# Optimization experiments

Hardware: AMD Instinct MI355X
Metric: run time of the kernel (lower is better)

## Reference

```python
import jax, jax.numpy as jnp
import numpy as np

N_LAYER, D_MODEL, D_INNER, D_STATE, DT_RANK, D_CONV = 4, 256, 512, 16, 16, 4
IN_FEAT, OUT_DIM, MID, NCLS, B, L = 64, 128, 50, 3, 16, 1024


def setup_inputs() -> dict:
    key = jax.random.key(0)
    ks = jax.random.split(key, 16)
    def lin(k, out_f, in_f, extra=()):  # stacked linear weights, fan_in scaled
        return jax.random.normal(k, extra + (out_f, in_f), jnp.float32) / np.sqrt(in_f)
    nl = (N_LAYER,)
    inp = {
        "x": jax.random.normal(ks[0], (B, L, IN_FEAT), jnp.float32),
        "emb_W": lin(ks[1], D_MODEL, IN_FEAT),
        "emb_b": jnp.zeros((D_MODEL,), jnp.float32),
        "in_W": lin(ks[2], 2 * D_INNER, D_MODEL, nl),
        "conv_W": jax.random.normal(ks[3], (N_LAYER, D_INNER, 1, D_CONV), jnp.float32) / np.sqrt(D_CONV),
        "conv_b": jnp.zeros((N_LAYER, D_INNER), jnp.float32),
        "xp_W": lin(ks[4], DT_RANK + 2 * D_STATE, D_INNER, nl),
        "dt_W": lin(ks[5], D_INNER, DT_RANK, nl),
        "dt_b": jnp.full((N_LAYER, D_INNER), -4.6, jnp.float32),  # softplus ~ 0.01
        "A_log": jnp.broadcast_to(jnp.log(jnp.arange(1, D_STATE + 1, dtype=jnp.float32)), (N_LAYER, D_INNER, D_STATE)),
        "Dp": jnp.ones((N_LAYER, D_INNER), jnp.float32),
        "out_W": lin(ks[6], D_MODEL, D_INNER, nl),
        "norm_W": jnp.ones((N_LAYER, D_MODEL), jnp.float32),
        "normf_W": jnp.ones((D_MODEL,), jnp.float32),
        "head_W": lin(ks[7], OUT_DIM, D_MODEL),
        "head_b": jnp.zeros((OUT_DIM,), jnp.float32),
        "W1": lin(ks[8], MID, OUT_DIM),
        "b1": jnp.zeros((MID,), jnp.float32),
        "W2": lin(ks[9], NCLS, MID),
        "b2": jnp.zeros((NCLS,), jnp.float32),
    }
    return inp


def _rmsnorm(x, w, eps=1e-5):
    return x * jax.lax.rsqrt(jnp.mean(x * x, axis=-1, keepdims=True) + eps) * w


def _causal_dwconv(x, w, b):  # x [B,L,D], w [D,1,K]
    xt = jnp.transpose(x, (0, 2, 1))  # [B,D,L]
    y = jax.lax.conv_general_dilated(
        xt, w, window_strides=(1,), padding=[(w.shape[-1] - 1, 0)],
        dimension_numbers=("NCH", "OIH", "NCH"), feature_group_count=xt.shape[1])
    return jnp.transpose(y, (0, 2, 1)) + b


def _selective_scan(dA, dBu, C):  # dA,dBu [B,L,D,N], C [B,L,N] -> y [B,L,D]
    dA_t = jnp.moveaxis(dA, 1, 0)
    dBu_t = jnp.moveaxis(dBu, 1, 0)
    C_t = jnp.moveaxis(C, 1, 0)
    h0 = jnp.zeros(dA.shape[:1] + dA.shape[2:], dA.dtype)  # [B,D,N]
    def step(h, inp):
        a, bu, c = inp
        h = a * h + bu
        return h, jnp.einsum("bdn,bn->bd", h, c)
    _, ys = jax.lax.scan(step, h0, (dA_t, dBu_t, C_t))
    return jnp.moveaxis(ys, 0, 1)


def _mamba_block(h, in_W, conv_W, conv_b, xp_W, dt_W, dt_b, A_log, Dp, out_W):
    xr = jnp.einsum("bld,ed->ble", h, in_W)  # [B,L,2*D_INNER]
    xm, res = jnp.split(xr, 2, axis=-1)
    xs = jax.nn.silu(_causal_dwconv(xm, conv_W, conv_b))
    dbc = jnp.einsum("bld,ed->ble", xs, xp_W)
    dlt, Bm, Cm = jnp.split(dbc, [DT_RANK, DT_RANK + D_STATE], axis=-1)
    delta = jax.nn.softplus(jnp.einsum("blr,dr->bld", dlt, dt_W) + dt_b)  # [B,L,D]
    A = -jnp.exp(A_log)  # [D,N]
    dA = jnp.exp(jnp.einsum("bld,dn->bldn", delta, A))
    dBu = jnp.einsum("bld,bln,bld->bldn", delta, Bm, xs)
    y = _selective_scan(dA, dBu, Cm) + xs * Dp
    y = y * jax.nn.silu(res)
    return jnp.einsum("bld,ed->ble", y, out_W)


def reference(x, emb_W, emb_b, in_W, conv_W, conv_b, xp_W, dt_W, dt_b, A_log,
              Dp, out_W, norm_W, normf_W, head_W, head_b, W1, b1, W2, b2):
    h = jnp.einsum("blf,df->bld", x, emb_W) + emb_b  # project to d_model
    for i in range(N_LAYER):
        h = h + _mamba_block(_rmsnorm(h, norm_W[i]), in_W[i], conv_W[i], conv_b[i],
                             xp_W[i], dt_W[i], dt_b[i], A_log[i], Dp[i], out_W[i])
    h = _rmsnorm(h, normf_W)
    feat = jnp.mean(jnp.einsum("bld,od->blo", h, head_W) + head_b, axis=1)  # [B,out_dim]
    hid = jax.nn.relu(feat @ W1.T + b1)
    return hid @ W2.T + b2  # [B, class_num] logits
```

## Files before the change

### kernel.cpp

```cpp
#include <hip/hip_runtime.h>
#include <math.h>

#define NL 4
#define DM 256
#define DI 512
#define DSTATE 16
#define DTRANK 16
#define DCONV 4
#define IN_FEAT 64
#define OUT_DIM 128
#define MID 50
#define NCLS 3
#define BB 16
#define LL 1024
#define T_TOK (BB*LL)
#define CHUNK 32
#define NCH (LL/CHUNK)

typedef short bf8_t __attribute__((ext_vector_type(8)));
typedef float f32x4 __attribute__((ext_vector_type(4)));

__device__ __forceinline__ float silu_f(float x) {
    return x / (1.f + __expf(-x));
}
__device__ __forceinline__ float softplus_f(float x) {
    return (x > 20.f) ? x : log1pf(__expf(x));
}
__device__ __forceinline__ unsigned short f2bf_rne(float f) {
    unsigned int u = __float_as_uint(f);
    unsigned int r = (u + 0x7FFFu + ((u >> 16) & 1u)) >> 16;
    return (unsigned short)r;
}
__device__ __forceinline__ float bf2f(unsigned short s) {
    return __uint_as_float(((unsigned int)s) << 16);
}
__device__ __forceinline__ void split_bf(float v, unsigned short& hi, unsigned short& lo) {
    unsigned short h = f2bf_rne(v);
    hi = h;
    lo = f2bf_rne(v - bf2f(h));
}
__device__ __forceinline__ void glds16(const unsigned short* g, unsigned short* l) {
    __builtin_amdgcn_global_load_lds(
        (const __attribute__((address_space(1))) void*)g,
        (__attribute__((address_space(3))) void*)l, 16, 0, 0);
}

template<int ACT, bool ACC, bool BIAS, bool SPLIT>
__global__ __launch_bounds__(256, 2)
void gemm_bf16x3(const unsigned short* __restrict__ Ahi,
                 const unsigned short* __restrict__ Alo,
                 const unsigned short* __restrict__ Whi,
                 const unsigned short* __restrict__ Wlo,
                 const float* __restrict__ bias,
                 float* __restrict__ C0, int ldc0,
                 float* __restrict__ C1, int ldc1, int NS,
                 int M, int N, int K)
{
    __shared__ __align__(16) unsigned short lds[4][128][32];

    const int tid = threadIdx.x;
    const int lane = tid & 63;
    const int bm = blockIdx.y * 128;
    const int bn = blockIdx.x * 128;
    const int wid = tid >> 6;
    const int wr = wid >> 1;
    const int wc = wid & 1;

    f32x4 acc[4][4];
    #pragma unroll
    for (int i = 0; i < 4; ++i)
        #pragma unroll
        for (int j = 0; j < 4; ++j)
            acc[i][j] = (f32x4){0.f, 0.f, 0.f, 0.f};

    const int l15 = lane & 15;
    const int kc  = lane >> 4;

    const int u0 = tid, u1 = tid + 256;
    const int r0 = u0 >> 2, s0 = (u0 & 3) ^ ((u0 >> 3) & 3);
    const int r1 = u1 >> 2, s1 = (u1 & 3) ^ ((u1 >> 3) & 3);

    for (int k0 = 0; k0 < K; k0 += 32) {
        __syncthreads();
        {
            const size_t ga0 = (size_t)(bm + r0) * K + k0 + s0 * 8;
            const size_t ga1 = (size_t)(bm + r1) * K + k0 + s1 * 8;
            const size_t gb0 = (size_t)(bn + r0) * K + k0 + s0 * 8;
            const size_t gb1 = (size_t)(bn + r1) * K + k0 + s1 * 8;
            glds16(Ahi + ga0, &lds[0][0][0] + u0 * 8);
            glds16(Ahi + ga1, &lds[0][0][0] + u1 * 8);
            glds16(Alo + ga0, &lds[1][0][0] + u0 * 8);
            glds16(Alo + ga1, &lds[1][0][0] + u1 * 8);
            glds16(Whi + gb0, &lds[2][0][0] + u0 * 8);
            glds16(Whi + gb1, &lds[2][0][0] + u1 * 8);
            glds16(Wlo + gb0, &lds[3][0][0] + u0 * 8);
            glds16(Wlo + gb1, &lds[3][0][0] + u1 * 8);
        }
        asm volatile("s_waitcnt vmcnt(0)" ::: "memory");
        __syncthreads();

        bf8_t ah[4], al[4], bh[4], bl[4];
        #pragma unroll
        for (int mi = 0; mi < 4; ++mi) {
            const int r = wr * 64 + mi * 16 + l15;
            const int sl = kc ^ ((r >> 1) & 3);
            ah[mi] = *(bf8_t*)&lds[0][r][sl * 8];
            al[mi] = *(bf8_t*)&lds[1][r][sl * 8];
        }
        #pragma unroll
        for (int nj = 0; nj < 4; ++nj) {
            const int r = wc * 64 + nj * 16 + l15;
            const int sl = kc ^ ((r >> 1) & 3);
            bh[nj] = *(bf8_t*)&lds[2][r][sl * 8];
            bl[nj] = *(bf8_t*)&lds[3][r][sl * 8];
        }

        #pragma unroll
        for (int mi = 0; mi < 4; ++mi)
            #pragma unroll
            for (int nj = 0; nj < 4; ++nj) {
                acc[mi][nj] = __builtin_amdgcn_mfma_f32_16x16x32_bf16(
                    ah[mi], bh[nj], acc[mi][nj], 0, 0, 0);
                acc[mi][nj] = __builtin_amdgcn_mfma_f32_16x16x32_bf16(
                    ah[mi], bl[nj], acc[mi][nj], 0, 0, 0);
                acc[mi][nj] = __builtin_amdgcn_mfma_f32_16x16x32_bf16(
                    al[mi], bh[nj], acc[mi][nj], 0, 0, 0);
            }
    }

    #pragma unroll
    for (int mi = 0; mi < 4; ++mi) {
        const int row0 = bm + wr * 64 + mi * 16 + (lane >> 4) * 4;
        #pragma unroll
        for (int nj = 0; nj < 4; ++nj) {
            const int col = bn + wc * 64 + nj * 16 + l15;
            float bv = BIAS ? bias[col] : 0.f;
            #pragma unroll
            for (int r = 0; r < 4; ++r) {
                float val = acc[mi][nj][r] + bv;
                if (ACT == 1) val = softplus_f(val);
                const int m = row0 + r;
                float* dst;
                if (SPLIT && col >= NS) dst = C1 + (size_t)m * ldc1 + (col - NS);
                else                    dst = C0 + (size_t)m * ldc0 + col;
                if (ACC) *dst += val; else *dst = val;
            }
        }
    }
}

__global__ __launch_bounds__(256, 2)
void gemm_bf16x3_bc(const unsigned short* __restrict__ Ahi,
                    const unsigned short* __restrict__ Alo,
                    const unsigned short* __restrict__ Whi,
                    const unsigned short* __restrict__ Wlo,
                    float* __restrict__ C, int K)
{
    __shared__ __align__(16) unsigned short ldsA[2][128][32];
    __shared__ __align__(16) unsigned short ldsW[2][48][32];

    const int tid = threadIdx.x;
    const int lane = tid & 63;
    const int wid = tid >> 6;
    const int bm = blockIdx.x * 128;

    f32x4 acc[2][3];
    #pragma unroll
    for (int i = 0; i < 2; ++i)
        #pragma unroll
        for (int j = 0; j < 3; ++j)
            acc[i][j] = (f32x4){0.f, 0.f, 0.f, 0.f};

    const int l15 = lane & 15;
    const int kc  = lane >> 4;

    const int u0 = tid, u1 = tid + 256;
    const int r0 = u0 >> 2, s0 = (u0 & 3) ^ ((u0 >> 3) & 3);
    const int r1 = u1 >> 2, s1 = (u1 & 3) ^ ((u1 >> 3) & 3);

    for (int k0 = 0; k0 < K; k0 += 32) {
        __syncthreads();
        {
            const size_t ga0 = (size_t)(bm + r0) * K + k0 + s0 * 8;
            const size_t ga1 = (size_t)(bm + r1) * K + k0 + s1 * 8;
            glds16(Ahi + ga0, &ldsA[0][0][0] + u0 * 8);
            glds16(Ahi + ga1, &ldsA[0][0][0] + u1 * 8);
            glds16(Alo + ga0, &ldsA[1][0][0] + u0 * 8);
            glds16(Alo + ga1, &ldsA[1][0][0] + u1 * 8);
            if (tid < 192) {
                const size_t gw = (size_t)r0 * K + k0 + s0 * 8;
                glds16(Whi + gw, &ldsW[0][0][0] + u0 * 8);
                glds16(Wlo + gw, &ldsW[1][0][0] + u0 * 8);
            }
        }
        asm volatile("s_waitcnt vmcnt(0)" ::: "memory");
        __syncthreads();

        bf8_t ah[2], al[2], bh[3], bl[3];
        #pragma unroll
        for (int mi = 0; mi < 2; ++mi) {
            const int r = wid * 32 + mi * 16 + l15;
            const int sl = kc ^ ((r >> 1) & 3);
            ah[mi] = *(bf8_t*)&ldsA[0][r][sl * 8];
            al[mi] = *(bf8_t*)&ldsA[1][r][sl * 8];
        }
        #pragma unroll
        for (int nj = 0; nj < 3; ++nj) {
            const int r = nj * 16 + l15;
            const int sl = kc ^ ((r >> 1) & 3);
            bh[nj] = *(bf8_t*)&ldsW[0][r][sl * 8];
            bl[nj] = *(bf8_t*)&ldsW[1][r][sl * 8];
        }

        #pragma unroll
        for (int mi = 0; mi < 2; ++mi)
            #pragma unroll
            for (int nj = 0; nj < 3; ++nj) {
                acc[mi][nj] = __builtin_amdgcn_mfma_f32_16x16x32_bf16(
                    ah[mi], bh[nj], acc[mi][nj], 0, 0, 0);
                acc[mi][nj] = __builtin_amdgcn_mfma_f32_16x16x32_bf16(
                    ah[mi], bl[nj], acc[mi][nj], 0, 0, 0);
                acc[mi][nj] = __builtin_amdgcn_mfma_f32_16x16x32_bf16(
                    al[mi], bh[nj], acc[mi][nj], 0, 0, 0);
            }
    }

    #pragma unroll
    for (int mi = 0; mi < 2; ++mi) {
        const int row0 = bm + wid * 32 + mi * 16 + (lane >> 4) * 4;
        #pragma unroll
        for (int nj = 0; nj < 3; ++nj) {
            const int col = nj * 16 + l15;
            #pragma unroll
            for (int r = 0; r < 4; ++r)
                C[(size_t)(row0 + r) * 48 + col] = acc[mi][nj][r];
        }
    }
}

__global__ __launch_bounds__(256)
void delta_kernel(const float* __restrict__ dbc, const float* __restrict__ dt_W,
                  const float* __restrict__ dt_b, float* __restrict__ delta)
{
    const int t = blockIdx.x;
    __shared__ float dl[16];
    if (threadIdx.x < 16) dl[threadIdx.x] = dbc[(size_t)t * 48 + threadIdx.x];
    __syncthreads();
    #pragma unroll
    for (int i = 0; i < 2; ++i) {
        const int d = threadIdx.x + i * 256;
        float s = dt_b[d];
        #pragma unroll
        for (int r = 0; r < 16; ++r)
            s = fmaf(dl[r], dt_W[d * 16 + r], s);
        delta[(size_t)t * DI + d] = softplus_f(s);
    }
}

template<int ACT, bool ACC>
__global__ __launch_bounds__(256)
void gemm_f32(const float* __restrict__ A, int lda,
              const float* __restrict__ Bw,
              const float* __restrict__ bias,
              float* __restrict__ C0, int ldc0,
              float* __restrict__ C1, int ldc1, int NS,
              int M, int N, int K)
{
    __shared__ float As[64][16];
    __shared__ float Bs[16][65];

    const int tid = threadIdx.x;
    const int bm = blockIdx.y * 64;
    const int bn = blockIdx.x * 64;
    const int tx = tid & 15;
    const int ty = tid >> 4;

    float acc[4][4] = {};

    const int r  = tid >> 2;
    const int kk = (tid & 3) * 4;

    for (int k0 = 0; k0 < K; k0 += 16) {
        int ar = bm + r; if (ar >= M) ar = M - 1;
        float4 av = *(const float4*)(A + (size_t)ar * lda + k0 + kk);
        *(float4*)(&As[r][kk]) = av;

        int br = bn + r; if (br >= N) br = N - 1;
        float4 bv = *(const float4*)(Bw + (size_t)br * K + k0 + kk);
        Bs[kk + 0][r] = bv.x;
        Bs[kk + 1][r] = bv.y;
        Bs[kk + 2][r] = bv.z;
        Bs[kk + 3][r] = bv.w;

        __syncthreads();
        #pragma unroll
        for (int k = 0; k < 16; ++k) {
            float a[4], bvv[4];
            #pragma unroll
            for (int i = 0; i < 4; ++i) a[i] = As[ty * 4 + i][k];
            #pragma unroll
            for (int j = 0; j < 4; ++j) bvv[j] = Bs[k][tx * 4 + j];
            #pragma unroll
            for (int i = 0; i < 4; ++i)
                #pragma unroll
                for (int j = 0; j < 4; ++j)
                    acc[i][j] = fmaf(a[i], bvv[j], acc[i][j]);
        }
        __syncthreads();
    }

    #pragma unroll
    for (int i = 0; i < 4; ++i) {
        int m = bm + ty * 4 + i;
        if (m >= M) continue;
        #pragma unroll
        for (int j = 0; j < 4; ++j) {
            int n = bn + tx * 4 + j;
            if (n >= N) continue;
            float v = acc[i][j];
            if (bias) v += bias[n];
            if (ACT == 1) v = softplus_f(v);
            float* dst;
            if (n < NS) dst = C0 + (size_t)m * ldc0 + n;
            else        dst = C1 + (size_t)m * ldc1 + (n - NS);
            if (ACC) *dst += v; else *dst = v;
        }
    }
}

__global__ __launch_bounds__(256)
void split4_kernel(const float* __restrict__ src, unsigned short* __restrict__ hi,
                   unsigned short* __restrict__ lo, int n4)
{
    int i = blockIdx.x * 256 + threadIdx.x;
    if (i >= n4) return;
    float4 v = ((const float4*)src)[i];
    ushort4 h, l;
    split_bf(v.x, h.x, l.x);
    split_bf(v.y, h.y, l.y);
    split_bf(v.z, h.z, l.z);
    split_bf(v.w, h.w, l.w);
    ((ushort4*)hi)[i] = h;
    ((ushort4*)lo)[i] = l;
}

__global__ __launch_bounds__(256)
void rmsnorm_bf16_kernel(const float* __restrict__ x, const float* __restrict__ w,
                         unsigned short* __restrict__ hi, unsigned short* __restrict__ lo)
{
    const int wave = threadIdx.x >> 6;
    const int lane = threadIdx.x & 63;
    const int t = blockIdx.x * 4 + wave;
    const float* xp = x + (size_t)t * DM;
    float4 v = *(const float4*)(xp + lane * 4);
    float ss = v.x * v.x + v.y * v.y + v.z * v.z + v.w * v.w;
    #pragma unroll
    for (int off = 1; off < 64; off <<= 1) ss += __shfl_xor(ss, off);
    float inv = rsqrtf(ss * (1.f / DM) + 1e-5f);
    float4 wv = *(const float4*)(w + lane * 4);
    float o[4] = { v.x * inv * wv.x, v.y * inv * wv.y,
                   v.z * inv * wv.z, v.w * inv * wv.w };
    ushort4 h, l;
    split_bf(o[0], h.x, l.x);
    split_bf(o[1], h.y, l.y);
    split_bf(o[2], h.z, l.z);
    split_bf(o[3], h.w, l.w);
    *(ushort4*)(hi + (size_t)t * DM + lane * 4) = h;
    *(ushort4*)(lo + (size_t)t * DM + lane * 4) = l;
}

__global__ __launch_bounds__(256)
void rmsnorm_kernel(const float* __restrict__ x, const float* __restrict__ w,
                    float* __restrict__ out)
{
    const int wave = threadIdx.x >> 6;
    const int lane = threadIdx.x & 63;
    const int t = blockIdx.x * 4 + wave;
    const float* xp = x + (size_t)t * DM;
    float4 v = *(const float4*)(xp + lane * 4);
    float ss = v.x * v.x + v.y * v.y + v.z * v.z + v.w * v.w;
    #pragma unroll
    for (int off = 1; off < 64; off <<= 1) ss += __shfl_xor(ss, off);
    float inv = rsqrtf(ss * (1.f / DM) + 1e-5f);
    float4 wv = *(const float4*)(w + lane * 4);
    float4 o;
    o.x = v.x * inv * wv.x;
    o.y = v.y * inv * wv.y;
    o.z = v.z * inv * wv.z;
    o.w = v.w * inv * wv.w;
    *(float4*)(out + (size_t)t * DM + lane * 4) = o;
}

__global__ __launch_bounds__(256)
void conv_silu_kernel(const float* __restrict__ xm,
                      const float* __restrict__ w,
                      const float* __restrict__ cb,
                      float* __restrict__ xs,
                      unsigned short* __restrict__ xs_hi,
                      unsigned short* __restrict__ xs_lo)
{
    const int idx = blockIdx.x * 256 + threadIdx.x;
    const int d = idx & (DI - 1);
    const int t = idx >> 9;
    const int l = t & (LL - 1);
    float acc = cb[d];
    const float* wp = w + d * 4;
    #pragma unroll
    for (int k = 0; k < 4; ++k) {
        int ll = l + k - 3;
        if (ll >= 0) acc = fmaf(xm[(size_t)(t + k - 3) * DI + d], wp[k], acc);
    }
    float v = silu_f(acc);
    xs[idx] = v;
    unsigned short hh, lo;
    split_bf(v, hh, lo);
    xs_hi[idx] = hh;
    xs_lo[idx] = lo;
}

__global__ __launch_bounds__(256)
void scan_p1(const float* __restrict__ delta,
             const float* __restrict__ dbc,
             const float* __restrict__ xs,
             const float* __restrict__ A_log,
             float* __restrict__ st,
             float* __restrict__ sdl)
{
    const int blk = blockIdx.x;
    const int dhalf = blk & 1;
    const int chunk = (blk >> 1) & (NCH - 1);
    const int b = blk >> 6;
    const int d = (dhalf << 8) + threadIdx.x;
    const int t0 = b * LL + chunk * CHUNK;

    __shared__ float Bs[CHUNK][DSTATE];
    for (int i = threadIdx.x; i < CHUNK * DSTATE; i += 256) {
        int s = i >> 4, n = i & 15;
        Bs[s][n] = dbc[(size_t)(t0 + s) * 48 + 16 + n];
    }
    __syncthreads();

    float An[16];
    #pragma unroll
    for (int n = 0; n < 16; ++n) An[n] = -__expf(A_log[d * 16 + n]);

    float h[16];
    #pragma unroll
    for (int n = 0; n < 16; ++n) h[n] = 0.f;
    float sumdl = 0.f;

    for (int s = 0; s < CHUNK; ++s) {
        const size_t off = (size_t)(t0 + s) * DI + d;
        const float dl = delta[off];
        const float du = dl * xs[off];
        sumdl += dl;
        #pragma unroll
        for (int n = 0; n < 16; ++n) {
            float a = __expf(dl * An[n]);
            h[n] = fmaf(a, h[n], du * Bs[s][n]);
        }
    }

    const size_t base = ((size_t)(b * NCH + chunk) * DSTATE) * DI + d;
    #pragma unroll
    for (int n = 0; n < 16; ++n) st[base + (size_t)n * DI] = h[n];
    sdl[(size_t)(b * NCH + chunk) * DI + d] = sumdl;
}

__global__ __launch_bounds__(256)
void scan_p2(float* __restrict__ st, const float* __restrict__ sdl,
             const float* __restrict__ A_log)
{
    const int b = blockIdx.x >> 1;
    const int d = ((blockIdx.x & 1) << 8) + threadIdx.x;

    float An[16];
    #pragma unroll
    for (int n = 0; n < 16; ++n) An[n] = -__expf(A_log[d * 16 + n]);

    float H[16];
    #pragma unroll
    for (int n = 0; n < 16; ++n) H[n] = 0.f;

    for (int c = 0; c < NCH; ++c) {
        const size_t base = ((size_t)(b * NCH + c) * DSTATE) * DI + d;
        const float sums = sdl[(size_t)(b * NCH + c) * DI + d];
        #pragma unroll
        for (int n = 0; n < 16; ++n) {
            float fin = st[base + (size_t)n * DI];
            float dec = __expf(An[n] * sums);
            st[base + (size_t)n * DI] = H[n];
            H[n] = fmaf(dec, H[n], fin);
        }
    }
}

__global__ __launch_bounds__(256)
void scan_p3(const float* __restrict__ delta,
             const float* __restrict__ dbc,
             const float* __restrict__ xs,
             const float* __restrict__ res,
             const float* __restrict__ A_log,
             const float* __restrict__ Dp,
             const float* __restrict__ st,
             unsigned short* __restrict__ y_hi,
             unsigned short* __restrict__ y_lo)
{
    const int blk = blockIdx.x;
    const int dhalf = blk & 1;
    const int chunk = (blk >> 1) & (NCH - 1);
    const int b = blk >> 6;
    const int d = (dhalf << 8) + threadIdx.x;
    const int t0 = b * LL + chunk * CHUNK;

    __shared__ float BCs[CHUNK][32];
    for (int i = threadIdx.x; i < CHUNK * 32; i += 256) {
        int s = i >> 5, c = i & 31;
        BCs[s][c] = dbc[(size_t)(t0 + s) * 48 + 16 + c];
    }
    __syncthreads();

    float An[16];
    #pragma unroll
    for (int n = 0; n < 16; ++n) An[n] = -__expf(A_log[d * 16 + n]);
    const float Dv = Dp[d];

    const size_t base = ((size_t)(b * NCH + chunk) * DSTATE) * DI + d;
    float h[16];
    #pragma unroll
    for (int n = 0; n < 16; ++n) h[n] = st[base + (size_t)n * DI];

    for (int s = 0; s < CHUNK; ++s) {
        const size_t off = (size_t)(t0 + s) * DI + d;
        const float dl = delta[off];
        const float xv = xs[off];
        const float rv = res[off];
        const float du = dl * xv;
        float acc = 0.f;
        #pragma unroll
        for (int n = 0; n < 16; ++n) {
            float a = __expf(dl * An[n]);
            h[n] = fmaf(a, h[n], du * BCs[s][n]);
            acc  = fmaf(h[n], BCs[s][16 + n], acc);
        }
        float y = fmaf(xv, Dv, acc) * silu_f(rv);
        unsigned short hh, ll;
        split_bf(y, hh, ll);
        y_hi[off] = hh;
        y_lo[off] = ll;
    }
}

__global__ void zero_kernel(float* __restrict__ p, int n)
{
    int i = blockIdx.x * 256 + threadIdx.x;
    if (i < n) p[i] = 0.f;
}

__global__ __launch_bounds__(256)
void hmean_kernel(const float* __restrict__ hn, float* __restrict__ hmean)
{
    const int b = blockIdx.x >> 4;
    const int lc = blockIdx.x & 15;
    const int d = threadIdx.x;
    float s = 0.f;
    for (int l = lc * 64; l < lc * 64 + 64; ++l)
        s += hn[((size_t)(b * LL + l)) * DM + d];
    atomicAdd(&hmean[b * DM + d], s * (1.f / LL));
}

__global__ __launch_bounds__(256)
void mlp_kernel(const float* __restrict__ feat, const float* __restrict__ W1,
                const float* __restrict__ b1, const float* __restrict__ W2,
                const float* __restrict__ b2, float* __restrict__ out)
{
    __shared__ float hid[BB][MID + 2];
    const int tid = threadIdx.x;
    for (int idx = tid; idx < BB * MID; idx += 256) {
        int b = idx / MID, m = idx % MID;
        float s = b1[m];
        for (int k = 0; k < OUT_DIM; ++k)
            s = fmaf(feat[b * OUT_DIM + k], W1[m * OUT_DIM + k], s);
        hid[b][m] = fmaxf(s, 0.f);
    }
    __syncthreads();
    if (tid < BB * NCLS) {
        int b = tid / NCLS, c = tid % NCLS;
        float s = b2[c];
        for (int k = 0; k < MID; ++k)
            s = fmaf(hid[b][k], W2[c * MID + k], s);
        out[b * NCLS + c] = s;
    }
}

extern "C" void kernel_launch(void* const* d_in, const int* in_sizes, int n_in,
                              void* d_out, int out_size, void* d_ws, size_t ws_size,
                              hipStream_t stream)
{
    const float* x       = (const float*)d_in[0];
    const float* emb_W   = (const float*)d_in[1];
    const float* emb_b   = (const float*)d_in[2];
    const float* in_W    = (const float*)d_in[3];
    const float* conv_W  = (const float*)d_in[4];
    const float* conv_b  = (const float*)d_in[5];
    const float* xp_W    = (const float*)d_in[6];
    const float* dt_W    = (const float*)d_in[7];
    const float* dt_b    = (const float*)d_in[8];
    const float* A_log   = (const float*)d_in[9];
    const float* Dp      = (const float*)d_in[10];
    const float* out_W   = (const float*)d_in[11];
    const float* norm_W  = (const float*)d_in[12];
    const float* normf_W = (const float*)d_in[13];
    const float* head_W  = (const float*)d_in[14];
    const float* head_b  = (const float*)d_in[15];
    const float* W1      = (const float*)d_in[16];
    const float* b1      = (const float*)d_in[17];
    const float* W2      = (const float*)d_in[18];
    const float* b2      = (const float*)d_in[19];

    const size_t TM = (size_t)T_TOK * DM;
    const size_t TD = (size_t)T_TOK * DI;

    float* ws    = (float*)d_ws;
    float* h     = ws;
    float* hn    = h   + TM;
    float* xm    = hn  + TM;
    float* res   = xm  + TD;
    float* xs    = res + TD;
    float* dbc   = xs  + TD;
    float* sdl   = dbc + (size_t)T_TOK * 48;
    float* hmean = sdl + (size_t)BB * NCH * DI;
    float* feat  = hmean + BB * DM;
    float* planes = feat + BB * OUT_DIM;
    float* wplanes = planes + TD;

    float* delta = xm;
    float* st  = hn;

    unsigned short* y_hi  = (unsigned short*)planes;
    unsigned short* y_lo  = y_hi + TD;
    unsigned short* xs_hi = (unsigned short*)planes;
    unsigned short* xs_lo = xs_hi + TD;
    unsigned short* hn_hi = (unsigned short*)planes;
    unsigned short* hn_lo = hn_hi + TM;
    unsigned short* x_hi  = (unsigned short*)planes;
    unsigned short* x_lo  = x_hi + (size_t)T_TOK * IN_FEAT;

    unsigned short* wp      = (unsigned short*)wplanes;
    unsigned short* embW_hi = wp;
    unsigned short* embW_lo = embW_hi + (size_t)DM * IN_FEAT;
    unsigned short* inW_hi  = embW_lo + (size_t)DM * IN_FEAT;
    unsigned short* inW_lo  = inW_hi + (size_t)NL * 2 * DI * DM;
    unsigned short* outW_hi = inW_lo + (size_t)NL * 2 * DI * DM;
    unsigned short* outW_lo = outW_hi + (size_t)NL * DM * DI;
    unsigned short* xpW_hi  = outW_lo + (size_t)NL * DM * DI;
    unsigned short* xpW_lo  = xpW_hi + (size_t)NL * 48 * DI;

    dim3 blk(256);

    split4_kernel<<<(DM * IN_FEAT / 4 + 255) / 256, blk, 0, stream>>>(
        emb_W, embW_hi, embW_lo, DM * IN_FEAT / 4);
    split4_kernel<<<(NL * 2 * DI * DM / 4 + 255) / 256, blk, 0, stream>>>(
        in_W, inW_hi, inW_lo, NL * 2 * DI * DM / 4);
    split4_kernel<<<(NL * DM * DI / 4 + 255) / 256, blk, 0, stream>>>(
        out_W, outW_hi, outW_lo, NL * DM * DI / 4);
    split4_kernel<<<(NL * 48 * DI / 4 + 255) / 256, blk, 0, stream>>>(
        xp_W, xpW_hi, xpW_lo, NL * 48 * DI / 4);
    split4_kernel<<<(T_TOK * IN_FEAT / 4 + 255) / 256, blk, 0, stream>>>(
        x, x_hi, x_lo, T_TOK * IN_FEAT / 4);

    gemm_bf16x3<0, false, true, false><<<dim3(DM / 128, T_TOK / 128), blk, 0, stream>>>(
        x_hi, x_lo, embW_hi, embW_lo, emb_b,
        h, DM, h, DM, DM, T_TOK, DM, IN_FEAT);

    for (int i = 0; i < NL; ++i) {
        rmsnorm_bf16_kernel<<<T_TOK / 4, blk, 0, stream>>>(
            h, norm_W + i * DM, hn_hi, hn_lo);

        gemm_bf16x3<0, false, false, true><<<dim3(2 * DI / 128, T_TOK / 128), blk, 0, stream>>>(
            hn_hi, hn_lo,
            inW_hi + (size_t)i * 2 * DI * DM, inW_lo + (size_t)i * 2 * DI * DM,
            nullptr, xm, DI, res, DI, DI, T_TOK, 2 * DI, DM);

        conv_silu_kernel<<<(T_TOK * DI) / 256, blk, 0, stream>>>(
            xm, conv_W + (size_t)i * DI * DCONV, conv_b + i * DI, xs, xs_hi, xs_lo);

        gemm_bf16x3_bc<<<T_TOK / 128, blk, 0, stream>>>(
            xs_hi, xs_lo, xpW_hi + (size_t)i * 48 * DI, xpW_lo + (size_t)i * 48 * DI,
            dbc, DI);

        delta_kernel<<<T_TOK, blk, 0, stream>>>(
            dbc, dt_W + (size_t)i * DI * DTRANK, dt_b + i * DI, delta);

        const float* Al = A_log + (size_t)i * DI * DSTATE;
        scan_p1<<<BB * NCH * 2, blk, 0, stream>>>(delta, dbc, xs, Al, st, sdl);
        scan_p2<<<32, blk, 0, stream>>>(st, sdl, Al);
        scan_p3<<<BB * NCH * 2, blk, 0, stream>>>(delta, dbc, xs, res, Al,
                                                  Dp + i * DI, st, y_hi, y_lo);

        gemm_bf16x3<0, true, false, false><<<dim3(DM / 128, T_TOK / 128), blk, 0, stream>>>(
            y_hi, y_lo,
            outW_hi + (size_t)i * DM * DI, outW_lo + (size_t)i * DM * DI,
            nullptr, h, DM, h, DM, DM, T_TOK, DM, DI);
    }

    rmsnorm_kernel<<<T_TOK / 4, blk, 0, stream>>>(h, normf_W, hn);
    zero_kernel<<<(BB * DM + 255) / 256, blk, 0, stream>>>(hmean, BB * DM);
    hmean_kernel<<<256, blk, 0, stream>>>(hn, hmean);
    gemm_f32<0, false><<<dim3(2, 1), blk, 0, stream>>>(
        hmean, DM, head_W, head_b, feat, OUT_DIM, feat, OUT_DIM, OUT_DIM,
        BB, OUT_DIM, DM);
    mlp_kernel<<<1, blk, 0, stream>>>(feat, W1, b1, W2, b2, (float*)d_out);
}
```

Before: 1.216 ms.

## Fuse delta projection into scan kernels and drop fp32 xs buffer

```diff
diff --git a/kernel.cpp b/kernel.cpp
--- a/kernel.cpp
+++ b/kernel.cpp
@@ -16,6 +16,7 @@
 #define T_TOK (BB*LL)
 #define CHUNK 32
 #define NCH (LL/CHUNK)
+#define TCH 16
 
 typedef short bf8_t __attribute__((ext_vector_type(8)));
 typedef float f32x4 __attribute__((ext_vector_type(4)));
@@ -238,25 +239,6 @@
     }
 }
 
-__global__ __launch_bounds__(256)
-void delta_kernel(const float* __restrict__ dbc, const float* __restrict__ dt_W,
-                  const float* __restrict__ dt_b, float* __restrict__ delta)
-{
-    const int t = blockIdx.x;
-    __shared__ float dl[16];
-    if (threadIdx.x < 16) dl[threadIdx.x] = dbc[(size_t)t * 48 + threadIdx.x];
-    __syncthreads();
-    #pragma unroll
-    for (int i = 0; i < 2; ++i) {
-        const int d = threadIdx.x + i * 256;
-        float s = dt_b[d];
-        #pragma unroll
-        for (int r = 0; r < 16; ++r)
-            s = fmaf(dl[r], dt_W[d * 16 + r], s);
-        delta[(size_t)t * DI + d] = softplus_f(s);
-    }
-}
-
 template<int ACT, bool ACC>
 __global__ __launch_bounds__(256)
 void gemm_f32(const float* __restrict__ A, int lda,
@@ -395,34 +377,53 @@
 void conv_silu_kernel(const float* __restrict__ xm,
                       const float* __restrict__ w,
                       const float* __restrict__ cb,
-                      float* __restrict__ xs,
                       unsigned short* __restrict__ xs_hi,
                       unsigned short* __restrict__ xs_lo)
 {
-    const int idx = blockIdx.x * 256 + threadIdx.x;
-    const int d = idx & (DI - 1);
-    const int t = idx >> 9;
-    const int l = t & (LL - 1);
-    float acc = cb[d];
-    const float* wp = w + d * 4;
-    #pragma unroll
-    for (int k = 0; k < 4; ++k) {
-        int ll = l + k - 3;
-        if (ll >= 0) acc = fmaf(xm[(size_t)(t + k - 3) * DI + d], wp[k], acc);
-    }
-    float v = silu_f(acc);
-    xs[idx] = v;
-    unsigned short hh, lo;
-    split_bf(v, hh, lo);
-    xs_hi[idx] = hh;
-    xs_lo[idx] = lo;
-}
-
-__global__ __launch_bounds__(256)
-void scan_p1(const float* __restrict__ delta,
-             const float* __restrict__ dbc,
-             const float* __restrict__ xs,
+    const int t0 = blockIdx.x * TCH;
+    const int l0 = t0 & (LL - 1);
+    const int d0 = threadIdx.x * 2;
+
+    const float4 wa = *(const float4*)(w + (size_t)d0 * 4);
+    const float4 wb = *(const float4*)(w + (size_t)(d0 + 1) * 4);
+    const float cbA = cb[d0], cbB = cb[d0 + 1];
+
+    float2 x0, x1, x2;
+    if (l0) {
+        x0 = *(const float2*)(xm + (size_t)(t0 - 3) * DI + d0);
+        x1 = *(const float2*)(xm + (size_t)(t0 - 2) * DI + d0);
+        x2 = *(const float2*)(xm + (size_t)(t0 - 1) * DI + d0);
+    } else {
+        x0 = x1 = x2 = (float2){0.f, 0.f};
+    }
+
+    #pragma unroll
+    for (int s = 0; s < TCH; ++s) {
+        const int t = t0 + s;
+        const float2 x3 = *(const float2*)(xm + (size_t)t * DI + d0);
+        float aA = cbA, aB = cbB;
+        aA = fmaf(wa.x, x0.x, aA); aB = fmaf(wb.x, x0.y, aB);
+        aA = fmaf(wa.y, x1.x, aA); aB = fmaf(wb.y, x1.y, aB);
+        aA = fmaf(wa.z, x2.x, aA); aB = fmaf(wb.z, x2.y, aB);
+        aA = fmaf(wa.w, x3.x, aA); aB = fmaf(wb.w, x3.y, aB);
+        const float vA = silu_f(aA);
+        const float vB = silu_f(aB);
+        ushort2 h2, l2;
+        split_bf(vA, h2.x, l2.x);
+        split_bf(vB, h2.y, l2.y);
+        *(ushort2*)(xs_hi + (size_t)t * DI + d0) = h2;
+        *(ushort2*)(xs_lo + (size_t)t * DI + d0) = l2;
+        x0 = x1; x1 = x2; x2 = x3;
+    }
+}
+
+__global__ __launch_bounds__(256)
+void scan_p1(const float* __restrict__ dbc,
+             const unsigned short* __restrict__ xs_hi,
+             const unsigned short* __restrict__ xs_lo,
              const float* __restrict__ A_log,
+             const float* __restrict__ dt_W,
+             const float* __restrict__ dt_b,
              float* __restrict__ st,
              float* __restrict__ sdl)
 {
@@ -433,16 +434,19 @@
     const int d = (dhalf << 8) + threadIdx.x;
     const int t0 = b * LL + chunk * CHUNK;
 
-    __shared__ float Bs[CHUNK][DSTATE];
-    for (int i = threadIdx.x; i < CHUNK * DSTATE; i += 256) {
-        int s = i >> 4, n = i & 15;
-        Bs[s][n] = dbc[(size_t)(t0 + s) * 48 + 16 + n];
+    __shared__ float Ls[CHUNK][32];
+    for (int i = threadIdx.x; i < CHUNK * 32; i += 256) {
+        int s = i >> 5, c = i & 31;
+        Ls[s][c] = dbc[(size_t)(t0 + s) * 48 + c];
     }
     __syncthreads();
 
-    float An[16];
+    float An[16], dtw[16];
     #pragma unroll
     for (int n = 0; n < 16; ++n) An[n] = -__expf(A_log[d * 16 + n]);
+    #pragma unroll
+    for (int r = 0; r < 16; ++r) dtw[r] = dt_W[d * 16 + r];
+    const float dtb = dt_b[d];
 
     float h[16];
     #pragma unroll
@@ -451,13 +455,17 @@
 
     for (int s = 0; s < CHUNK; ++s) {
         const size_t off = (size_t)(t0 + s) * DI + d;
-        const float dl = delta[off];
-        const float du = dl * xs[off];
+        float sp = dtb;
+        #pragma unroll
+        for (int r = 0; r < 16; ++r) sp = fmaf(Ls[s][r], dtw[r], sp);
+        const float dl = softplus_f(sp);
+        const float xv = bf2f(xs_hi[off]) + bf2f(xs_lo[off]);
+        const float du = dl * xv;
         sumdl += dl;
         #pragma unroll
         for (int n = 0; n < 16; ++n) {
             float a = __expf(dl * An[n]);
-            h[n] = fmaf(a, h[n], du * Bs[s][n]);
+            h[n] = fmaf(a, h[n], du * Ls[s][16 + n]);
         }
     }
 
@@ -496,11 +504,13 @@
 }
 
 __global__ __launch_bounds__(256)
-void scan_p3(const float* __restrict__ delta,
-             const float* __restrict__ dbc,
-             const float* __restrict__ xs,
+void scan_p3(const float* __restrict__ dbc,
+             const unsigned short* __restrict__ xs_hi,
+             const unsigned short* __restrict__ xs_lo,
              const float* __restrict__ res,
              const float* __restrict__ A_log,
+             const float* __restrict__ dt_W,
+             const float* __restrict__ dt_b,
              const float* __restrict__ Dp,
              const float* __restrict__ st,
              unsigned short* __restrict__ y_hi,
@@ -513,16 +523,19 @@
     const int d = (dhalf << 8) + threadIdx.x;
     const int t0 = b * LL + chunk * CHUNK;
 
-    __shared__ float BCs[CHUNK][32];
-    for (int i = threadIdx.x; i < CHUNK * 32; i += 256) {
-        int s = i >> 5, c = i & 31;
-        BCs[s][c] = dbc[(size_t)(t0 + s) * 48 + 16 + c];
+    __shared__ float Ls[CHUNK][48];
+    for (int i = threadIdx.x; i < CHUNK * 48; i += 256) {
+        int s = i / 48, c = i % 48;
+        Ls[s][c] = dbc[(size_t)(t0 + s) * 48 + c];
     }
     __syncthreads();
 
-    float An[16];
+    float An[16], dtw[16];
     #pragma unroll
     for (int n = 0; n < 16; ++n) An[n] = -__expf(A_log[d * 16 + n]);
+    #pragma unroll
+    for (int r = 0; r < 16; ++r) dtw[r] = dt_W[d * 16 + r];
+    const float dtb = dt_b[d];
     const float Dv = Dp[d];
 
     const size_t base = ((size_t)(b * NCH + chunk) * DSTATE) * DI + d;
@@ -532,16 +545,19 @@
 
     for (int s = 0; s < CHUNK; ++s) {
         const size_t off = (size_t)(t0 + s) * DI + d;
-        const float dl = delta[off];
-        const float xv = xs[off];
+        float sp = dtb;
+        #pragma unroll
+        for (int r = 0; r < 16; ++r) sp = fmaf(Ls[s][r], dtw[r], sp);
+        const float dl = softplus_f(sp);
+        const float xv = bf2f(xs_hi[off]) + bf2f(xs_lo[off]);
         const float rv = res[off];
         const float du = dl * xv;
         float acc = 0.f;
         #pragma unroll
         for (int n = 0; n < 16; ++n) {
             float a = __expf(dl * An[n]);
-            h[n] = fmaf(a, h[n], du * BCs[s][n]);
-            acc  = fmaf(h[n], BCs[s][16 + n], acc);
+            h[n] = fmaf(a, h[n], du * Ls[s][16 + n]);
+            acc  = fmaf(h[n], Ls[s][32 + n], acc);
         }
         float y = fmaf(xv, Dv, acc) * silu_f(rv);
         unsigned short hh, ll;
@@ -626,15 +642,14 @@
     float* hn    = h   + TM;
     float* xm    = hn  + TM;
     float* res   = xm  + TD;
-    float* xs    = res + TD;
-    float* dbc   = xs  + TD;
+    float* xs_unused = res + TD;
+    float* dbc   = xs_unused + TD;
     float* sdl   = dbc + (size_t)T_TOK * 48;
     float* hmean = sdl + (size_t)BB * NCH * DI;
     float* feat  = hmean + BB * DM;
     float* planes = feat + BB * OUT_DIM;
     float* wplanes = planes + TD;
 
-    float* delta = xm;
     float* st  = hn;
 
     unsigned short* y_hi  = (unsigned short*)planes;
@@ -674,6 +689,9 @@
         h, DM, h, DM, DM, T_TOK, DM, IN_FEAT);
 
     for (int i = 0; i < NL; ++i) {
+        const float* dtW_i = dt_W + (size_t)i * DI * DTRANK;
+        const float* dtb_i = dt_b + i * DI;
+
         rmsnorm_bf16_kernel<<<T_TOK / 4, blk, 0, stream>>>(
             h, norm_W + i * DM, hn_hi, hn_lo);
 
@@ -682,21 +700,19 @@
             inW_hi + (size_t)i * 2 * DI * DM, inW_lo + (size_t)i * 2 * DI * DM,
             nullptr, xm, DI, res, DI, DI, T_TOK, 2 * DI, DM);
 
-        conv_silu_kernel<<<(T_TOK * DI) / 256, blk, 0, stream>>>(
-            xm, conv_W + (size_t)i * DI * DCONV, conv_b + i * DI, xs, xs_hi, xs_lo);
+        conv_silu_kernel<<<T_TOK / TCH, blk, 0, stream>>>(
+            xm, conv_W + (size_t)i * DI * DCONV, conv_b + i * DI, xs_hi, xs_lo);
 
         gemm_bf16x3_bc<<<T_TOK / 128, blk, 0, stream>>>(
             xs_hi, xs_lo, xpW_hi + (size_t)i * 48 * DI, xpW_lo + (size_t)i * 48 * DI,
             dbc, DI);
 
-        delta_kernel<<<T_TOK, blk, 0, stream>>>(
-            dbc, dt_W + (size_t)i * DI * DTRANK, dt_b + i * DI, delta);
-
         const float* Al = A_log + (size_t)i * DI * DSTATE;
-        scan_p1<<<BB * NCH * 2, blk, 0, stream>>>(delta, dbc, xs, Al, st, sdl);
+        scan_p1<<<BB * NCH * 2, blk, 0, stream>>>(
+            dbc, xs_hi, xs_lo, Al, dtW_i, dtb_i, st, sdl);
         scan_p2<<<32, blk, 0, stream>>>(st, sdl, Al);
-        scan_p3<<<BB * NCH * 2, blk, 0, stream>>>(delta, dbc, xs, res, Al,
-                                                  Dp + i * DI, st, y_hi, y_lo);
+        scan_p3<<<BB * NCH * 2, blk, 0, stream>>>(
+            dbc, xs_hi, xs_lo, res, Al, dtW_i, dtb_i, Dp + i * DI, st, y_hi, y_lo);
 
         gemm_bf16x3<0, true, false, false><<<dim3(DM / 128, T_TOK / 128), blk, 0, stream>>>(
             y_hi, y_lo,
```

Result: no change. 1.211 ms (-0.4%).
